# Optimization experiments

Measured on AMD Instinct MI355X. Metric: run time of the kernel, lower is better.

The kernel has to match this reference:

```python
import jax, jax.numpy as jnp
import numpy as np

B, A, L, D, H = 8, 16, 80, 128, 6  # scenes, agents/scene, lanes/scene, feat dim, heads
LN_EPS = 1e-5


def _build_edges():
    hi_l, wi_l = [], []
    n_agt = B * A
    for b in range(B):
        ids = np.concatenate([np.arange(b * A, (b + 1) * A),
                              n_agt + np.arange(b * L, (b + 1) * L)])
        n = len(ids)
        hi_l.append(np.repeat(ids, n))  # 'd -> (d n)'
        wi_l.append(np.tile(ids, n))    # 'd -> (n d)'
    return (jnp.asarray(np.concatenate(hi_l), dtype=jnp.int32),
            jnp.asarray(np.concatenate(wi_l), dtype=jnp.int32))


def setup_inputs() -> dict:
    key = jax.random.key(0)
    ks = jax.random.split(key, 10)
    w = 0.05  # small init so exp(att) is well-behaved
    hi, wi = _build_edges()
    return {
        "agents": jax.random.normal(ks[0], (B * A, D), jnp.float32),
        "lanes": jax.random.normal(ks[1], (B * L, D), jnp.float32),
        "Wq": w * jax.random.normal(ks[2], (D, H * D), jnp.float32),
        "Wk": w * jax.random.normal(ks[3], (D, H * D), jnp.float32),
        "Wv": w * jax.random.normal(ks[4], (D, H * D), jnp.float32),
        "Wout1": w * jax.random.normal(ks[5], (H * D, D), jnp.float32),
        "Wout2": w * jax.random.normal(ks[6], (D, D), jnp.float32),
        "W1": w * jax.random.normal(ks[7], (D, D), jnp.float32),
        "ln_g": jnp.ones((D,), jnp.float32),
        "ln_b": jnp.zeros((D,), jnp.float32),
        "W2": w * jax.random.normal(ks[8], (D, D), jnp.float32),
        "hi": hi,
        "wi": wi,
    }


def _layernorm(x, g, b):
    mu = x.mean(-1, keepdims=True)
    var = ((x - mu) ** 2).mean(-1, keepdims=True)
    return (x - mu) * jax.lax.rsqrt(var + LN_EPS) * g + b


def reference(agents, lanes, Wq, Wk, Wv, Wout1, Wout2, W1, ln_g, ln_b, W2, hi, wi):
    nodes = jnp.concatenate([agents, lanes], axis=0)  # [N, D]
    N = nodes.shape[0]
    n_agt = agents.shape[0]
    scale = D ** -0.5

    src = nodes[hi]  # [E, D] (query side)
    dst = nodes[wi]  # [E, D] (key/value side)
    q = (src @ Wq).reshape(-1, H, D)
    k = (dst @ Wk).reshape(-1, H, D)
    v = jax.nn.relu(dst @ Wv).reshape(-1, H, D)

    att = jnp.einsum('ehd,ehd->eh', q, k) * scale          # [E, H]
    att = jnp.exp(att - att.max())                          # global-max-shifted exp (as in source)
    denom = jax.ops.segment_sum(att, hi, num_segments=N)    # [N, H]
    att = att / denom[hi]
    out = jax.ops.segment_sum(att[..., None] * v, hi, num_segments=N)  # [N, H, D]
    out = out.reshape(N, H * D)

    out = jax.nn.relu(out @ Wout1) @ Wout2                  # to_out
    h = _layernorm(nodes @ W1 + out, ln_g, ln_b)
    h = jax.nn.relu(h)
    h = h @ W2
    h = jax.nn.relu(h + nodes)                              # residual to pre-attention nodes
    return h[:n_agt]
```

## Files before the change

### kernel.cpp

```cpp
#include <hip/hip_runtime.h>
#include <math.h>

#define LN_EPS 1e-5f


__global__ __launch_bounds__(512) void k_attn_all(
    const float* __restrict__ agents, const float* __restrict__ lanes,
    const float* __restrict__ Wq, const float* __restrict__ Wk,
    const float* __restrict__ Wv, float* __restrict__ AO)
{
    __shared__ float Ns[96][132];
    __shared__ float Vh[96][68];
    __shared__ float Qs[16][132];
    __shared__ float Tt[16][132];
    __shared__ float Sm[16][100];
    __shared__ float Wc[64][132];

    const int tid = threadIdx.x;
    const int b = blockIdx.x;
    const int s = b / 12, r12 = b % 12;
    const int h = r12 >> 1, half = r12 & 1;

    #pragma unroll
    for (int ii = 0; ii < 6; ++ii) {
        const int idx = tid + ii * 512;
        const int n = idx >> 5, c4 = idx & 31;
        const float* src = (n < 16) ? (agents + (size_t)(s * 16 + n) * 128)
                                    : (lanes + (size_t)(s * 80 + n - 16) * 128);
        *(float4*)&Ns[n][c4 * 4] = *(const float4*)(src + c4 * 4);
    }

    const int r = tid >> 5, jc = tid & 31;

    float q0 = 0, q1 = 0, q2 = 0, q3 = 0;
    for (int ck = 0; ck < 2; ++ck) {
        __syncthreads();
        #pragma unroll
        for (int ii = 0; ii < 4; ++ii) {
            const int idx = tid + ii * 512;
            const int row = idx >> 5, c4 = idx & 31;
            *(float4*)&Wc[row][c4 * 4] =
                *(const float4*)(Wq + (size_t)(ck * 64 + row) * 768 + h * 128 + c4 * 4);
        }
        __syncthreads();
        #pragma unroll 4
        for (int kk = 0; kk < 64; ++kk) {
            const float a = Ns[r][ck * 64 + kk];
            q0 += a * Wc[kk][jc];
            q1 += a * Wc[kk][jc + 32];
            q2 += a * Wc[kk][jc + 64];
            q3 += a * Wc[kk][jc + 96];
        }
    }
    Qs[r][jc] = q0; Qs[r][jc + 32] = q1; Qs[r][jc + 64] = q2; Qs[r][jc + 96] = q3;

    const int rg = tid >> 4, cv = tid & 15;
    float4 va0 = make_float4(0,0,0,0), va1 = va0, va2 = va0;
    for (int ck = 0; ck < 2; ++ck) {
        __syncthreads();
        #pragma unroll
        for (int ii = 0; ii < 2; ++ii) {
            const int idx = tid + ii * 512;
            const int row = idx >> 4, cc = idx & 15;
            *(float4*)&Wc[row][cc * 4] =
                *(const float4*)(Wv + (size_t)(ck * 64 + row) * 768 +
                                 h * 128 + half * 64 + cc * 4);
        }
        __syncthreads();
        #pragma unroll 4
        for (int kk = 0; kk < 64; ++kk) {
            const float4 w = *(const float4*)&Wc[kk][cv * 4];
            const float n0 = Ns[rg][ck * 64 + kk];
            const float n1 = Ns[rg + 32][ck * 64 + kk];
            const float n2 = Ns[rg + 64][ck * 64 + kk];
            va0.x += n0 * w.x; va0.y += n0 * w.y; va0.z += n0 * w.z; va0.w += n0 * w.w;
            va1.x += n1 * w.x; va1.y += n1 * w.y; va1.z += n1 * w.z; va1.w += n1 * w.w;
            va2.x += n2 * w.x; va2.y += n2 * w.y; va2.z += n2 * w.z; va2.w += n2 * w.w;
        }
    }
    va0.x = fmaxf(va0.x, 0.f); va0.y = fmaxf(va0.y, 0.f);
    va0.z = fmaxf(va0.z, 0.f); va0.w = fmaxf(va0.w, 0.f);
    va1.x = fmaxf(va1.x, 0.f); va1.y = fmaxf(va1.y, 0.f);
    va1.z = fmaxf(va1.z, 0.f); va1.w = fmaxf(va1.w, 0.f);
    va2.x = fmaxf(va2.x, 0.f); va2.y = fmaxf(va2.y, 0.f);
    va2.z = fmaxf(va2.z, 0.f); va2.w = fmaxf(va2.w, 0.f);
    *(float4*)&Vh[rg][cv * 4]      = va0;
    *(float4*)&Vh[rg + 32][cv * 4] = va1;
    *(float4*)&Vh[rg + 64][cv * 4] = va2;

    for (int ck = 0; ck < 2; ++ck) {
        __syncthreads();
        #pragma unroll
        for (int ii = 0; ii < 4; ++ii) {
            const int idx = tid + ii * 512;
            const int row = idx >> 5, c4 = idx & 31;
            *(float4*)&Wc[row][c4 * 4] =
                *(const float4*)(Wk + (size_t)(ck * 64 + row) * 768 + h * 128 + c4 * 4);
        }
        __syncthreads();
        float a1 = 0, a2 = 0;
        #pragma unroll 4
        for (int c4i = 0; c4i < 32; ++c4i) {
            const float4 q  = *(const float4*)&Qs[r][c4i * 4];
            const float4 w1 = *(const float4*)&Wc[jc][c4i * 4];
            const float4 w2 = *(const float4*)&Wc[jc + 32][c4i * 4];
            a1 += q.x * w1.x + q.y * w1.y + q.z * w1.z + q.w * w1.w;
            a2 += q.x * w2.x + q.y * w2.y + q.z * w2.z + q.w * w2.w;
        }
        Tt[r][ck * 64 + jc]      = a1;
        Tt[r][ck * 64 + 32 + jc] = a2;
    }
    __syncthreads();

    {
        const int i = r;
        float s0 = 0, s1 = 0, s2 = 0;
        #pragma unroll 4
        for (int kk = 0; kk < 32; ++kk) {
            const float4 t4 = *(const float4*)&Tt[i][kk * 4];
            const float4 a  = *(const float4*)&Ns[jc][kk * 4];
            const float4 bb = *(const float4*)&Ns[jc + 32][kk * 4];
            const float4 c  = *(const float4*)&Ns[jc + 64][kk * 4];
            s0 += t4.x*a.x  + t4.y*a.y  + t4.z*a.z  + t4.w*a.w;
            s1 += t4.x*bb.x + t4.y*bb.y + t4.z*bb.z + t4.w*bb.w;
            s2 += t4.x*c.x  + t4.y*c.y  + t4.z*c.z  + t4.w*c.w;
        }
        const float scale = 0.088388347648318447f;
        s0 *= scale; s1 *= scale; s2 *= scale;
        float m = fmaxf(fmaxf(s0, s1), s2);
        #pragma unroll
        for (int o = 16; o >= 1; o >>= 1) m = fmaxf(m, __shfl_xor(m, o, 32));
        const float e0 = __expf(s0 - m), e1 = __expf(s1 - m), e2 = __expf(s2 - m);
        float sum = e0 + e1 + e2;
        #pragma unroll
        for (int o = 16; o >= 1; o >>= 1) sum += __shfl_xor(sum, o, 32);
        const float inv = 1.0f / sum;
        Sm[i][jc]      = e0 * inv;
        Sm[i][jc + 32] = e1 * inv;
        Sm[i][jc + 64] = e2 * inv;
    }

    {
        const int i = r, d = jc;
        float o0 = 0, o1 = 0;
        #pragma unroll 4
        for (int j = 0; j < 96; ++j) {
            const float p = Sm[i][j];
            const float2 v = *(const float2*)&Vh[j][2 * d];
            o0 += p * v.x; o1 += p * v.y;
        }
        float* dst = AO + (size_t)(s * 16 + i) * 768 + h * 128 + half * 64 + 2 * d;
        *(float2*)dst = make_float2(o0, o1);
    }
}

__global__ __launch_bounds__(512) void k_tail(
    const float* __restrict__ AO, const float* __restrict__ agents,
    const float* __restrict__ Wout1, const float* __restrict__ Wout2,
    const float* __restrict__ W1, const float* __restrict__ ln_g,
    const float* __restrict__ ln_b, const float* __restrict__ W2,
    float* __restrict__ out)
{
    const int a = blockIdx.x;
    const int tid = threadIdx.x;
    __shared__ float AOs[768];
    __shared__ float nr[128];
    __shared__ float y1s[128];
    __shared__ float hb[128];
    __shared__ float ps[512];
    __shared__ float red[4];

    if (tid < 192) {
        *(float4*)&AOs[tid * 4] = *(const float4*)(AO + (size_t)a * 768 + tid * 4);
    } else if (tid < 224) {
        const int t = tid - 192;
        *(float4*)&nr[t * 4] = *(const float4*)(agents + (size_t)a * 128 + t * 4);
    }
    __syncthreads();

    const int d = tid & 127, g = tid >> 7;

    {
        const int k0 = g * 192;
        float p = 0.f;
        #pragma unroll 8
        for (int k = 0; k < 192; ++k)
            p += AOs[k0 + k] * Wout1[(size_t)(k0 + k) * 128 + d];
        ps[tid] = p;
    }
    __syncthreads();
    if (tid < 128) y1s[d] = fmaxf(ps[d] + ps[128 + d] + ps[256 + d] + ps[384 + d], 0.f);
    __syncthreads();

    {
        const float* src = (g < 2) ? y1s : nr;
        const float* Wm  = (g < 2) ? Wout2 : W1;
        const int k0 = (g & 1) * 64;
        float p = 0.f;
        #pragma unroll 8
        for (int k = 0; k < 64; ++k)
            p += src[k0 + k] * Wm[(size_t)(k0 + k) * 128 + d];
        ps[tid] = p;
    }
    __syncthreads();

    float tval = 0.f;
    if (tid < 128) tval = ps[d] + ps[128 + d] + ps[256 + d] + ps[384 + d];
    float s1 = tval, s2 = tval * tval;
    #pragma unroll
    for (int o = 32; o >= 1; o >>= 1) { s1 += __shfl_xor(s1, o); s2 += __shfl_xor(s2, o); }
    if (tid < 128 && (tid & 63) == 0) {
        red[(tid >> 6) * 2] = s1; red[(tid >> 6) * 2 + 1] = s2;
    }
    __syncthreads();
    if (tid < 128) {
        const float S1 = red[0] + red[2], S2 = red[1] + red[3];
        const float mu  = S1 * (1.0f / 128.0f);
        const float var = S2 * (1.0f / 128.0f) - mu * mu;
        const float rin = rsqrtf(var + LN_EPS);
        hb[d] = fmaxf((tval - mu) * rin * ln_g[d] + ln_b[d], 0.0f);
    }
    __syncthreads();

    {
        const int k0 = g * 32;
        float p = 0.f;
        #pragma unroll 8
        for (int k = 0; k < 32; ++k)
            p += hb[k0 + k] * W2[(size_t)(k0 + k) * 128 + d];
        ps[tid] = p;
    }
    __syncthreads();
    if (tid < 128)
        out[(size_t)a * 128 + d] =
            fmaxf(ps[d] + ps[128 + d] + ps[256 + d] + ps[384 + d] + nr[d], 0.0f);
}

extern "C" void kernel_launch(void* const* d_in, const int* in_sizes, int n_in,
                              void* d_out, int out_size, void* d_ws, size_t ws_size,
                              hipStream_t stream)
{
    const float* agents = (const float*)d_in[0];
    const float* lanes  = (const float*)d_in[1];
    const float* Wq     = (const float*)d_in[2];
    const float* Wk     = (const float*)d_in[3];
    const float* Wv     = (const float*)d_in[4];
    const float* Wout1  = (const float*)d_in[5];
    const float* Wout2  = (const float*)d_in[6];
    const float* W1     = (const float*)d_in[7];
    const float* ln_g   = (const float*)d_in[8];
    const float* ln_b   = (const float*)d_in[9];
    const float* W2     = (const float*)d_in[10];

    float* AO   = (float*)d_ws;
    float* outp = (float*)d_out;

    k_attn_all<<<96, 512, 0, stream>>>(agents, lanes, Wq, Wk, Wv, AO);
    k_tail    <<<128, 512, 0, stream>>>(AO, agents, Wout1, Wout2, W1,
                                        ln_g, ln_b, W2, outp);
}
```

Before: 112.7 us.

## Split Q/K/V projections into a separate tiled GEMM kernel ahead of attention

Moves the Q, K and V projections out of the per-(scene, head, half) attention blocks into a new 312-block tiled GEMM kernel. That kernel writes V (with ReLU), K and Q for all nodes to workspace. The attention kernel then just loads the precomputed K/V/Q slices, and the K projection is applied directly to the keys instead of being folded into the query through Wk transposed. This targets the serial projection work done inside only 96 blocks, and it spreads the GEMMs over more blocks. The cost is an extra kernel launch and a round trip of about 5 MB through global memory.

```diff
diff --git a/kernel.cpp b/kernel.cpp
--- a/kernel.cpp
+++ b/kernel.cpp
@@ -4,126 +4,132 @@
 #define LN_EPS 1e-5f
 
 
-__global__ __launch_bounds__(512) void k_attn_all(
+__global__ __launch_bounds__(256) void k_qkv(
     const float* __restrict__ agents, const float* __restrict__ lanes,
-    const float* __restrict__ Wq, const float* __restrict__ Wk,
-    const float* __restrict__ Wv, float* __restrict__ AO)
-{
-    __shared__ float Ns[96][132];
+    const float* __restrict__ Wv, const float* __restrict__ Wk,
+    const float* __restrict__ Wq, float* __restrict__ V,
+    float* __restrict__ Kb, float* __restrict__ Qb)
+{
+    __shared__ float As[128][68];
+    __shared__ float Bs[128][68];
+
+    const int tid = threadIdx.x;
+    const int bid = blockIdx.x;
+
+    const float* W;
+    float* Out;
+    int r0, wc0;
+    bool dorelu = false;
+    if (bid < 144) {
+        const int rb = bid % 12, cb = bid / 12;
+        r0 = rb * 64; W = Wv; wc0 = cb * 64; Out = V; dorelu = true;
+    } else if (bid < 288) {
+        const int idx = bid - 144;
+        const int rb = idx % 12, cb = idx / 12;
+        r0 = rb * 64; W = Wk; wc0 = cb * 64; Out = Kb;
+    } else {
+        const int idx = bid - 288;
+        r0 = (idx & 1) * 64; W = Wq; wc0 = (idx >> 1) * 64; Out = Qb;
+    }
+
+    {
+        const int row = tid >> 2, kv = tid & 3;
+        const int gr = r0 + row;
+        const float* src = (gr < 128) ? (agents + (size_t)gr * 128)
+                                      : (lanes + (size_t)(gr - 128) * 128);
+        #pragma unroll
+        for (int j = 0; j < 8; ++j) {
+            const int k0 = kv * 4 + j * 16;
+            const float4 a = *(const float4*)(src + k0);
+            As[k0 + 0][row] = a.x; As[k0 + 1][row] = a.y;
+            As[k0 + 2][row] = a.z; As[k0 + 3][row] = a.w;
+        }
+    }
+    {
+        const int kr = tid >> 4, c4 = tid & 15;
+        #pragma unroll
+        for (int i = 0; i < 8; ++i) {
+            const int k = kr + 16 * i;
+            *(float4*)&Bs[k][c4 * 4] =
+                *(const float4*)(W + (size_t)k * 768 + wc0 + c4 * 4);
+        }
+    }
+    __syncthreads();
+
+    const int tx = tid & 15, ty = tid >> 4;
+    float acc[4][4] = {};
+    #pragma unroll 8
+    for (int k = 0; k < 128; ++k) {
+        const float4 a = *(const float4*)&As[k][ty * 4];
+        const float4 b = *(const float4*)&Bs[k][tx * 4];
+        const float av[4] = {a.x, a.y, a.z, a.w};
+        #pragma unroll
+        for (int i = 0; i < 4; ++i) {
+            acc[i][0] += av[i] * b.x; acc[i][1] += av[i] * b.y;
+            acc[i][2] += av[i] * b.z; acc[i][3] += av[i] * b.w;
+        }
+    }
+    #pragma unroll
+    for (int i = 0; i < 4; ++i) {
+        float4 v = make_float4(acc[i][0], acc[i][1], acc[i][2], acc[i][3]);
+        if (dorelu) {
+            v.x = fmaxf(v.x, 0.f); v.y = fmaxf(v.y, 0.f);
+            v.z = fmaxf(v.z, 0.f); v.w = fmaxf(v.w, 0.f);
+        }
+        *(float4*)(Out + (size_t)(r0 + ty * 4 + i) * 768 + wc0 + tx * 4) = v;
+    }
+}
+
+__global__ __launch_bounds__(512) void k_attn3(
+    const float* __restrict__ Kb, const float* __restrict__ V,
+    const float* __restrict__ Qb, float* __restrict__ AO)
+{
+    __shared__ float Ks[96][136];
     __shared__ float Vh[96][68];
     __shared__ float Qs[16][132];
-    __shared__ float Tt[16][132];
     __shared__ float Sm[16][100];
-    __shared__ float Wc[64][132];
 
     const int tid = threadIdx.x;
     const int b = blockIdx.x;
     const int s = b / 12, r12 = b % 12;
     const int h = r12 >> 1, half = r12 & 1;
 
+    {
+        const int r = tid >> 5, c4 = tid & 31;
+        *(float4*)&Qs[r][c4 * 4] =
+            *(const float4*)(Qb + (size_t)(s * 16 + r) * 768 + h * 128 + c4 * 4);
+    }
     #pragma unroll
     for (int ii = 0; ii < 6; ++ii) {
         const int idx = tid + ii * 512;
         const int n = idx >> 5, c4 = idx & 31;
-        const float* src = (n < 16) ? (agents + (size_t)(s * 16 + n) * 128)
-                                    : (lanes + (size_t)(s * 80 + n - 16) * 128);
-        *(float4*)&Ns[n][c4 * 4] = *(const float4*)(src + c4 * 4);
-    }
-
-    const int r = tid >> 5, jc = tid & 31;
-
-    float q0 = 0, q1 = 0, q2 = 0, q3 = 0;
-    for (int ck = 0; ck < 2; ++ck) {
-        __syncthreads();
-        #pragma unroll
-        for (int ii = 0; ii < 4; ++ii) {
-            const int idx = tid + ii * 512;
-            const int row = idx >> 5, c4 = idx & 31;
-            *(float4*)&Wc[row][c4 * 4] =
-                *(const float4*)(Wq + (size_t)(ck * 64 + row) * 768 + h * 128 + c4 * 4);
-        }
-        __syncthreads();
-        #pragma unroll 4
-        for (int kk = 0; kk < 64; ++kk) {
-            const float a = Ns[r][ck * 64 + kk];
-            q0 += a * Wc[kk][jc];
-            q1 += a * Wc[kk][jc + 32];
-            q2 += a * Wc[kk][jc + 64];
-            q3 += a * Wc[kk][jc + 96];
-        }
-    }
-    Qs[r][jc] = q0; Qs[r][jc + 32] = q1; Qs[r][jc + 64] = q2; Qs[r][jc + 96] = q3;
-
-    const int rg = tid >> 4, cv = tid & 15;
-    float4 va0 = make_float4(0,0,0,0), va1 = va0, va2 = va0;
-    for (int ck = 0; ck < 2; ++ck) {
-        __syncthreads();
-        #pragma unroll
-        for (int ii = 0; ii < 2; ++ii) {
-            const int idx = tid + ii * 512;
-            const int row = idx >> 4, cc = idx & 15;
-            *(float4*)&Wc[row][cc * 4] =
-                *(const float4*)(Wv + (size_t)(ck * 64 + row) * 768 +
-                                 h * 128 + half * 64 + cc * 4);
-        }
-        __syncthreads();
-        #pragma unroll 4
-        for (int kk = 0; kk < 64; ++kk) {
-            const float4 w = *(const float4*)&Wc[kk][cv * 4];
-            const float n0 = Ns[rg][ck * 64 + kk];
-            const float n1 = Ns[rg + 32][ck * 64 + kk];
-            const float n2 = Ns[rg + 64][ck * 64 + kk];
-            va0.x += n0 * w.x; va0.y += n0 * w.y; va0.z += n0 * w.z; va0.w += n0 * w.w;
-            va1.x += n1 * w.x; va1.y += n1 * w.y; va1.z += n1 * w.z; va1.w += n1 * w.w;
-            va2.x += n2 * w.x; va2.y += n2 * w.y; va2.z += n2 * w.z; va2.w += n2 * w.w;
-        }
-    }
-    va0.x = fmaxf(va0.x, 0.f); va0.y = fmaxf(va0.y, 0.f);
-    va0.z = fmaxf(va0.z, 0.f); va0.w = fmaxf(va0.w, 0.f);
-    va1.x = fmaxf(va1.x, 0.f); va1.y = fmaxf(va1.y, 0.f);
-    va1.z = fmaxf(va1.z, 0.f); va1.w = fmaxf(va1.w, 0.f);
-    va2.x = fmaxf(va2.x, 0.f); va2.y = fmaxf(va2.y, 0.f);
-    va2.z = fmaxf(va2.z, 0.f); va2.w = fmaxf(va2.w, 0.f);
-    *(float4*)&Vh[rg][cv * 4]      = va0;
-    *(float4*)&Vh[rg + 32][cv * 4] = va1;
-    *(float4*)&Vh[rg + 64][cv * 4] = va2;
-
-    for (int ck = 0; ck < 2; ++ck) {
-        __syncthreads();
-        #pragma unroll
-        for (int ii = 0; ii < 4; ++ii) {
-            const int idx = tid + ii * 512;
-            const int row = idx >> 5, c4 = idx & 31;
-            *(float4*)&Wc[row][c4 * 4] =
-                *(const float4*)(Wk + (size_t)(ck * 64 + row) * 768 + h * 128 + c4 * 4);
-        }
-        __syncthreads();
-        float a1 = 0, a2 = 0;
-        #pragma unroll 4
-        for (int c4i = 0; c4i < 32; ++c4i) {
-            const float4 q  = *(const float4*)&Qs[r][c4i * 4];
-            const float4 w1 = *(const float4*)&Wc[jc][c4i * 4];
-            const float4 w2 = *(const float4*)&Wc[jc + 32][c4i * 4];
-            a1 += q.x * w1.x + q.y * w1.y + q.z * w1.z + q.w * w1.w;
-            a2 += q.x * w2.x + q.y * w2.y + q.z * w2.z + q.w * w2.w;
-        }
-        Tt[r][ck * 64 + jc]      = a1;
-        Tt[r][ck * 64 + 32 + jc] = a2;
-    }
-    __syncthreads();
-
-    {
-        const int i = r;
+        const int g = (n < 16) ? (s * 16 + n) : (128 + s * 80 + (n - 16));
+        *(float4*)&Ks[n][c4 * 4] =
+            *(const float4*)(Kb + (size_t)g * 768 + h * 128 + c4 * 4);
+    }
+    #pragma unroll
+    for (int ii = 0; ii < 3; ++ii) {
+        const int idx = tid + ii * 512;
+        const int n = idx >> 4, c4 = idx & 15;
+        const int g = (n < 16) ? (s * 16 + n) : (128 + s * 80 + (n - 16));
+        *(float4*)&Vh[n][c4 * 4] =
+            *(const float4*)(V + (size_t)g * 768 + h * 128 + half * 64 + c4 * 4);
+    }
+    __syncthreads();
+
+    const int i = tid >> 5, jc = tid & 31;
+
+    {
         float s0 = 0, s1 = 0, s2 = 0;
         #pragma unroll 4
         for (int kk = 0; kk < 32; ++kk) {
-            const float4 t4 = *(const float4*)&Tt[i][kk * 4];
-            const float4 a  = *(const float4*)&Ns[jc][kk * 4];
-            const float4 bb = *(const float4*)&Ns[jc + 32][kk * 4];
-            const float4 c  = *(const float4*)&Ns[jc + 64][kk * 4];
-            s0 += t4.x*a.x  + t4.y*a.y  + t4.z*a.z  + t4.w*a.w;
-            s1 += t4.x*bb.x + t4.y*bb.y + t4.z*bb.z + t4.w*bb.w;
-            s2 += t4.x*c.x  + t4.y*c.y  + t4.z*c.z  + t4.w*c.w;
+            const float4 q  = *(const float4*)&Qs[i][kk * 4];
+            const float4 k0 = *(const float4*)&Ks[jc][kk * 4];
+            const float4 k1 = *(const float4*)&Ks[jc + 32][kk * 4];
+            const float4 k2 = *(const float4*)&Ks[jc + 64][kk * 4];
+            s0 += q.x*k0.x + q.y*k0.y + q.z*k0.z + q.w*k0.w;
+            s1 += q.x*k1.x + q.y*k1.y + q.z*k1.z + q.w*k1.w;
+            s2 += q.x*k2.x + q.y*k2.y + q.z*k2.z + q.w*k2.w;
         }
         const float scale = 0.088388347648318447f;
         s0 *= scale; s1 *= scale; s2 *= scale;
@@ -141,7 +147,7 @@
     }
 
     {
-        const int i = r, d = jc;
+        const int d = jc;
         float o0 = 0, o1 = 0;
         #pragma unroll 4
         for (int j = 0; j < 96; ++j) {
@@ -252,10 +258,15 @@
     const float* ln_b   = (const float*)d_in[9];
     const float* W2     = (const float*)d_in[10];
 
-    float* AO   = (float*)d_ws;
+    float* ws = (float*)d_ws;
+    float* V    = ws;
+    float* Kb   = V + 768 * 768;
+    float* Qb   = Kb + 768 * 768;
+    float* AO   = Qb + 128 * 768;
     float* outp = (float*)d_out;
 
-    k_attn_all<<<96, 512, 0, stream>>>(agents, lanes, Wq, Wk, Wv, AO);
-    k_tail    <<<128, 512, 0, stream>>>(AO, agents, Wout1, Wout2, W1,
-                                        ln_g, ln_b, W2, outp);
-}
+    k_qkv  <<<312, 256, 0, stream>>>(agents, lanes, Wv, Wk, Wq, V, Kb, Qb);
+    k_attn3<<<96, 512, 0, stream>>>(Kb, V, Qb, AO);
+    k_tail <<<128, 512, 0, stream>>>(AO, agents, Wout1, Wout2, W1,
+                                     ln_g, ln_b, W2, outp);
+}
```

New measurement: 109.9 us. 2.5% less time.
